# Performance work log

Measured on AMD Instinct MI355X. Metric: run time of the kernel, lower is better.

Reference implementation:

```python
import jax, jax.numpy as jnp
import numpy as np

B, N, C, H = 16, 4096, 256, 4
D = C // H

def setup_inputs() -> dict:
    key = jax.random.key(0)
    ks = jax.random.split(key, 8)
    w = 0.01  # small init, mimics xavier_uniform gain=0.1
    x = jax.random.normal(ks[0], (B, N, C), jnp.float32)
    S = jax.random.normal(ks[1], (B, H, D, D), jnp.float32) * 0.1
    Wq = jax.random.normal(ks[2], (C, C), jnp.float32) * w
    Wk = jax.random.normal(ks[3], (C, C), jnp.float32) * w
    Wv = jax.random.normal(ks[4], (C, C), jnp.float32) * w
    Wb = jax.random.normal(ks[5], (H, C), jnp.float32) * w  # beta_proj (zeros in torch init; random for nontrivial math)
    Wo = jax.random.normal(ks[6], (C, C), jnp.float32) * w
    g_rms = jnp.ones((C,), jnp.float32)
    return {"x": x, "S": S, "Wq": Wq, "Wk": Wk, "Wv": Wv, "Wb": Wb, "Wo": Wo, "g_rms": g_rms}

def reference(x, S, Wq, Wk, Wv, Wb, Wo, g_rms):
    b, n, c = x.shape
    h = Wb.shape[0]
    d = c // h
    # projections -> (B,H,N,D)
    q = (x @ Wq.T).reshape(b, n, h, d).transpose(0, 2, 1, 3)
    k = (x @ Wk.T).reshape(b, n, h, d).transpose(0, 2, 1, 3)
    v = (x @ Wv.T).reshape(b, n, h, d).transpose(0, 2, 1, 3)
    # feature map + L2 normalize keys
    k = jax.nn.elu(k) + 1.0
    k = k / (jnp.linalg.norm(k, axis=-1, keepdims=True) + 1e-6)
    # per-head gates (B,H,N,1)
    beta = jax.nn.sigmoid(jnp.einsum('bnc,hc->bhn', x, Wb))[..., None]
    # decay + state read
    Sd = S * 0.95
    y = jnp.einsum('bhij,bhnj->bhni', Sd, q)
    pred = jnp.einsum('bhij,bhnj->bhni', Sd, k)
    # delta-rule write: outer(mean weighted error, mean key)
    w_err = jnp.mean(beta * (v - pred), axis=2)  # (B,H,D)
    w_key = jnp.mean(k, axis=2)                  # (B,H,D)
    S_new = jnp.clip(Sd + jnp.einsum('bhi,bhj->bhij', w_err, w_key), -10.0, 10.0)
    # merge heads, RMSNorm, output projection
    y = y.transpose(0, 2, 1, 3).reshape(b, n, c)
    y = y * jax.lax.rsqrt(jnp.mean(y * y, axis=-1, keepdims=True) + 1e-6) * g_rms
    out = y @ Wo.T
    return out, S_new
```

## Files before the change

kernel.cpp:

```cpp
#include <hip/hip_runtime.h>
#include <math.h>


typedef _Float16 f16;
typedef f16 f16x8 __attribute__((ext_vector_type(8)));
typedef f16 f16x4 __attribute__((ext_vector_type(4)));
typedef float f32x4 __attribute__((ext_vector_type(4)));

__device__ __forceinline__ f16x8 cvt8(const float* q) {
  float4 a = *(const float4*)q;
  float4 b = *(const float4*)(q + 4);
  f16x8 r;
  r[0] = (f16)a.x; r[1] = (f16)a.y; r[2] = (f16)a.z; r[3] = (f16)a.w;
  r[4] = (f16)b.x; r[5] = (f16)b.y; r[6] = (f16)b.z; r[7] = (f16)b.w;
  return r;
}

__global__ __launch_bounds__(256) void prep_w(
    const float* __restrict__ Wk, const float* __restrict__ Wo,
    const float* __restrict__ g, f16* __restrict__ Wkh,
    f16* __restrict__ Wogh) {
  int i = blockIdx.x * 256 + threadIdx.x;
#pragma unroll
  for (int j = 0; j < 4; ++j) {
    int idx = i + j * 16384;
    Wkh[idx] = (f16)Wk[idx];
    Wogh[idx] = (f16)(Wo[idx] * g[idx & 255]);
  }
}

__global__ __launch_bounds__(256) void beta_xbsum_h(
    const float* __restrict__ x, const float* __restrict__ Wb,
    float* __restrict__ betaArr, float* __restrict__ xbsum,
    f16* __restrict__ xh) {
  const int t = threadIdx.x;
  const int wave = t >> 6, lane = t & 63;
  const int b = blockIdx.x >> 6;
  const int tile = blockIdx.x & 63;
  float4 wb[4];
#pragma unroll
  for (int h = 0; h < 4; ++h) wb[h] = *(const float4*)(Wb + h * 256 + lane * 4);
  float xacc[4][4] = {};
  const size_t rowbase = (size_t)b * 4096 + tile * 64;
  __shared__ float bsh[4][64];
  float4 xv = *(const float4*)(x + (rowbase + wave) * 256 + lane * 4);
#pragma unroll 2
  for (int i = 0; i < 16; ++i) {
    int r = i * 4 + wave;
    float4 nx = xv;
    if (i < 15)
      nx = *(const float4*)(x + (rowbase + r + 4) * 256 + lane * 4);
    f16x4 hx;
    hx[0] = (f16)xv.x; hx[1] = (f16)xv.y; hx[2] = (f16)xv.z; hx[3] = (f16)xv.w;
    *(f16x4*)(xh + (rowbase + r) * 256 + lane * 4) = hx;
#pragma unroll
    for (int h = 0; h < 4; ++h) {
      float s = xv.x * wb[h].x + xv.y * wb[h].y + xv.z * wb[h].z + xv.w * wb[h].w;
#pragma unroll
      for (int off = 32; off; off >>= 1) s += __shfl_xor(s, off);
      float bh = 1.f / (1.f + __expf(-s));
      if (lane == h) bsh[h][r] = bh;
      xacc[h][0] += bh * xv.x; xacc[h][1] += bh * xv.y;
      xacc[h][2] += bh * xv.z; xacc[h][3] += bh * xv.w;
    }
    xv = nx;
  }
  __shared__ float xbp[4][4][256];
#pragma unroll
  for (int h = 0; h < 4; ++h)
#pragma unroll
    for (int j = 0; j < 4; ++j) xbp[wave][h][lane * 4 + j] = xacc[h][j];
  __syncthreads();
  {
    int h = t >> 6, r = t & 63;
    betaArr[((size_t)(b * 4 + h) << 12) + tile * 64 + r] = bsh[h][r];
  }
  for (int idx = t; idx < 1024; idx += 256) {
    int h = idx >> 8, c = idx & 255;
    float s = xbp[0][h][c] + xbp[1][h][c] + xbp[2][h][c] + xbp[3][h][c];
    atomicAdd(&xbsum[(b * 4 + h) * 256 + c], s);
  }
}

__global__ __launch_bounds__(256) void kgemm_h(
    const f16* __restrict__ xh, const f16* __restrict__ Wkh,
    const float* __restrict__ betaArr,
    float* __restrict__ ksum, float* __restrict__ kbsum) {
  __shared__ union {
    struct { f16 A[128][72]; f16 B[128][72]; } s;
    f16 K[128][132];
  } u;
  __shared__ float bstage[2][128];
  const int t = threadIdx.x;
  const int m0 = blockIdx.y * 128;
  const int n0 = blockIdx.x * 128;
  const int b = m0 >> 12;
  const int wave = t >> 6, lane = t & 63;
  const int wm = (wave >> 1) * 64, wn = (wave & 1) * 64;
  const int fr = lane & 15, fq = lane >> 4;
  {
    int hh = t >> 7, r = t & 127;
    bstage[hh][r] =
        betaArr[((size_t)(b * 4 + (n0 >> 6) + hh) << 12) + (m0 & 4095) + r];
  }
  f32x4 acc[4][4] = {};
#pragma unroll 1
  for (int kt = 0; kt < 4; ++kt) {
    const int k0 = kt * 64;
#pragma unroll
    for (int i = 0; i < 4; ++i) {
      int id = i * 256 + t;
      int row = id >> 3, cc = id & 7;
      *(uint4*)&u.s.A[row][cc * 8] =
          *(const uint4*)(xh + (size_t)(m0 + row) * 256 + k0 + cc * 8);
      *(uint4*)&u.s.B[row][cc * 8] =
          *(const uint4*)(Wkh + (size_t)(n0 + row) * 256 + k0 + cc * 8);
    }
    __syncthreads();
#pragma unroll
    for (int ks = 0; ks < 2; ++ks) {
      f16x8 afr[4], bfr[4];
#pragma unroll
      for (int mi = 0; mi < 4; ++mi)
        afr[mi] = *(const f16x8*)&u.s.A[wm + mi * 16 + fr][ks * 32 + fq * 8];
#pragma unroll
      for (int ni = 0; ni < 4; ++ni)
        bfr[ni] = *(const f16x8*)&u.s.B[wn + ni * 16 + fr][ks * 32 + fq * 8];
#pragma unroll
      for (int mi = 0; mi < 4; ++mi)
#pragma unroll
        for (int ni = 0; ni < 4; ++ni)
          acc[mi][ni] = __builtin_amdgcn_mfma_f32_16x16x32_f16(
              afr[mi], bfr[ni], acc[mi][ni], 0, 0, 0);
    }
    __syncthreads();
  }
#pragma unroll
  for (int mi = 0; mi < 4; ++mi)
#pragma unroll
    for (int rr = 0; rr < 4; ++rr) {
      float s = 0.f;
#pragma unroll
      for (int ni = 0; ni < 4; ++ni) {
        float v = acc[mi][ni][rr];
        v = v > 0.f ? v + 1.f : __expf(v);
        acc[mi][ni][rr] = v;
        s += v * v;
      }
#pragma unroll
      for (int off = 1; off < 16; off <<= 1) s += __shfl_xor(s, off);
      float inv = 1.f / (sqrtf(s) + 1e-6f);
#pragma unroll
      for (int ni = 0; ni < 4; ++ni) acc[mi][ni][rr] *= inv;
    }
#pragma unroll
  for (int mi = 0; mi < 4; ++mi)
#pragma unroll
    for (int ni = 0; ni < 4; ++ni)
#pragma unroll
      for (int rr = 0; rr < 4; ++rr)
        u.K[wm + mi * 16 + fq * 4 + rr][wn + ni * 16 + fr] = (f16)acc[mi][ni][rr];
  __syncthreads();
  if (t < 128) {
    const int c = t, hl = c >> 6;
    float sk = 0.f, skb = 0.f;
#pragma unroll 4
    for (int r = 0; r < 128; ++r) {
      float v = (float)u.K[r][c];
      float be = bstage[hl][r];
      sk += v;
      skb += be * v;
    }
    int gh = b * 4 + (n0 >> 6) + hl;
    atomicAdd(&ksum[gh * 64 + (c & 63)], sk);
    atomicAdd(&kbsum[gh * 64 + (c & 63)], skb);
  }
}

__global__ __launch_bounds__(256) void fold_M(
    const float* __restrict__ S, const float* __restrict__ Wq,
    f16* __restrict__ M) {
  const int bh = blockIdx.y;
  const int dq = blockIdx.x;
  const int h = bh & 3;
  const int t = threadIdx.x;
  const float* Sp = S + (size_t)bh * 4096 + dq * 8 * 64;
  const float* Wp = Wq + (size_t)h * 64 * 256 + t;
  float m[8] = {};
#pragma unroll 4
  for (int e = 0; e < 64; ++e) {
    float wv = Wp[e * 256];
#pragma unroll
    for (int dd = 0; dd < 8; ++dd) m[dd] += Sp[dd * 64 + e] * wv;
  }
  f16* Mb = M + (size_t)(bh >> 2) * 65536;
#pragma unroll
  for (int dd = 0; dd < 8; ++dd)
    Mb[(size_t)(h * 64 + dq * 8 + dd) * 256 + t] = (f16)(0.95f * m[dd]);
}

__global__ __launch_bounds__(256) void ygemm_h(
    const f16* __restrict__ xh, int m_base, const f16* __restrict__ M,
    f16* __restrict__ y, float* __restrict__ rowssq) {
  __shared__ f16 As[128][72];
  __shared__ f16 Bs[128][72];
  const int t = threadIdx.x;
  const int m0 = blockIdx.y * 128;
  const int n0 = blockIdx.x * 128;
  const int b = (m_base + m0) >> 12;
  const f16* Mb = M + (size_t)b * 65536;
  const int wave = t >> 6, lane = t & 63;
  const int wm = (wave >> 1) * 64, wn = (wave & 1) * 64;
  const int fr = lane & 15, fq = lane >> 4;
  f32x4 acc[4][4] = {};
#pragma unroll 1
  for (int kt = 0; kt < 4; ++kt) {
    const int k0 = kt * 64;
#pragma unroll
    for (int i = 0; i < 4; ++i) {
      int id = i * 256 + t;
      int row = id >> 3, cc = id & 7;
      *(uint4*)&As[row][cc * 8] =
          *(const uint4*)(xh + (size_t)(m_base + m0 + row) * 256 + k0 + cc * 8);
      *(uint4*)&Bs[row][cc * 8] =
          *(const uint4*)(Mb + (size_t)(n0 + row) * 256 + k0 + cc * 8);
    }
    __syncthreads();
#pragma unroll
    for (int ks = 0; ks < 2; ++ks) {
      f16x8 afr[4], bfr[4];
#pragma unroll
      for (int mi = 0; mi < 4; ++mi)
        afr[mi] = *(const f16x8*)&As[wm + mi * 16 + fr][ks * 32 + fq * 8];
#pragma unroll
      for (int ni = 0; ni < 4; ++ni)
        bfr[ni] = *(const f16x8*)&Bs[wn + ni * 16 + fr][ks * 32 + fq * 8];
#pragma unroll
      for (int mi = 0; mi < 4; ++mi)
#pragma unroll
        for (int ni = 0; ni < 4; ++ni)
          acc[mi][ni] = __builtin_amdgcn_mfma_f32_16x16x32_f16(
              afr[mi], bfr[ni], acc[mi][ni], 0, 0, 0);
    }
    __syncthreads();
  }
#pragma unroll
  for (int mi = 0; mi < 4; ++mi)
#pragma unroll
    for (int rr = 0; rr < 4; ++rr) {
      float s = 0.f;
#pragma unroll
      for (int ni = 0; ni < 4; ++ni) {
        float v = acc[mi][ni][rr];
        s += v * v;
        int row = m0 + wm + mi * 16 + fq * 4 + rr;
        int col = n0 + wn + ni * 16 + fr;
        y[(size_t)row * 256 + col] = (f16)v;
      }
#pragma unroll
      for (int off = 1; off < 16; off <<= 1) s += __shfl_xor(s, off);
      if (fr == 0)
        atomicAdd(&rowssq[m0 + wm + mi * 16 + fq * 4 + rr], s);
    }
}

__global__ __launch_bounds__(256) void ogemm_h(
    const f16* __restrict__ y, const float* __restrict__ rowssq,
    const f16* __restrict__ Wogh, float* __restrict__ out, int m_base) {
  __shared__ f16 As[128][72];
  __shared__ f16 Bs[128][72];
  __shared__ float rsl[128];
  const int t = threadIdx.x;
  const int m0 = blockIdx.y * 128;
  const int n0 = blockIdx.x * 128;
  const int wave = t >> 6, lane = t & 63;
  const int wm = (wave >> 1) * 64, wn = (wave & 1) * 64;
  const int fr = lane & 15, fq = lane >> 4;
  if (t < 128) rsl[t] = rsqrtf(rowssq[m0 + t] * (1.f / 256.f) + 1e-6f);
  f32x4 acc[4][4] = {};
#pragma unroll 1
  for (int kt = 0; kt < 4; ++kt) {
    const int k0 = kt * 64;
#pragma unroll
    for (int i = 0; i < 4; ++i) {
      int id = i * 256 + t;
      int row = id >> 3, cc = id & 7;
      *(uint4*)&As[row][cc * 8] =
          *(const uint4*)(y + (size_t)(m0 + row) * 256 + k0 + cc * 8);
      *(uint4*)&Bs[row][cc * 8] =
          *(const uint4*)(Wogh + (size_t)(n0 + row) * 256 + k0 + cc * 8);
    }
    __syncthreads();
#pragma unroll
    for (int ks = 0; ks < 2; ++ks) {
      f16x8 afr[4], bfr[4];
#pragma unroll
      for (int mi = 0; mi < 4; ++mi)
        afr[mi] = *(const f16x8*)&As[wm + mi * 16 + fr][ks * 32 + fq * 8];
#pragma unroll
      for (int ni = 0; ni < 4; ++ni)
        bfr[ni] = *(const f16x8*)&Bs[wn + ni * 16 + fr][ks * 32 + fq * 8];
#pragma unroll
      for (int mi = 0; mi < 4; ++mi)
#pragma unroll
        for (int ni = 0; ni < 4; ++ni)
          acc[mi][ni] = __builtin_amdgcn_mfma_f32_16x16x32_f16(
              afr[mi], bfr[ni], acc[mi][ni], 0, 0, 0);
    }
    __syncthreads();
  }
#pragma unroll
  for (int mi = 0; mi < 4; ++mi)
#pragma unroll
    for (int rr = 0; rr < 4; ++rr) {
      int lrow = wm + mi * 16 + fq * 4 + rr;
      float rs = rsl[lrow];
#pragma unroll
      for (int ni = 0; ni < 4; ++ni) {
        int row = m_base + m0 + lrow;
        int col = n0 + wn + ni * 16 + fr;
        out[(size_t)row * 256 + col] = rs * acc[mi][ni][rr];
      }
    }
}

__global__ __launch_bounds__(256) void beta_xbsum(
    const float* __restrict__ x, const float* __restrict__ Wb,
    float* __restrict__ betaArr, float* __restrict__ xbsum) {
  const int t = threadIdx.x;
  const int wave = t >> 6, lane = t & 63;
  const int b = blockIdx.x >> 6;
  const int tile = blockIdx.x & 63;
  float4 wb[4];
#pragma unroll
  for (int h = 0; h < 4; ++h) wb[h] = *(const float4*)(Wb + h * 256 + lane * 4);
  float xacc[4][4] = {};
  const size_t rowbase = (size_t)b * 4096 + tile * 64;
  __shared__ float bsh[4][64];
  float4 xv = *(const float4*)(x + (rowbase + wave) * 256 + lane * 4);
#pragma unroll 2
  for (int i = 0; i < 16; ++i) {
    int r = i * 4 + wave;
    float4 nx = xv;
    if (i < 15)
      nx = *(const float4*)(x + (rowbase + r + 4) * 256 + lane * 4);
#pragma unroll
    for (int h = 0; h < 4; ++h) {
      float s = xv.x * wb[h].x + xv.y * wb[h].y + xv.z * wb[h].z + xv.w * wb[h].w;
#pragma unroll
      for (int off = 32; off; off >>= 1) s += __shfl_xor(s, off);
      float bh = 1.f / (1.f + __expf(-s));
      if (lane == h) bsh[h][r] = bh;
      xacc[h][0] += bh * xv.x; xacc[h][1] += bh * xv.y;
      xacc[h][2] += bh * xv.z; xacc[h][3] += bh * xv.w;
    }
    xv = nx;
  }
  __shared__ float xbp[4][4][256];
#pragma unroll
  for (int h = 0; h < 4; ++h)
#pragma unroll
    for (int j = 0; j < 4; ++j) xbp[wave][h][lane * 4 + j] = xacc[h][j];
  __syncthreads();
  {
    int h = t >> 6, r = t & 63;
    betaArr[((size_t)(b * 4 + h) << 12) + tile * 64 + r] = bsh[h][r];
  }
  for (int idx = t; idx < 1024; idx += 256) {
    int h = idx >> 8, c = idx & 255;
    float s = xbp[0][h][c] + xbp[1][h][c] + xbp[2][h][c] + xbp[3][h][c];
    atomicAdd(&xbsum[(b * 4 + h) * 256 + c], s);
  }
}

__global__ __launch_bounds__(256) void kgemm_sums(
    const float* __restrict__ x, const float* __restrict__ Wk,
    const float* __restrict__ betaArr,
    float* __restrict__ ksum, float* __restrict__ kbsum) {
  __shared__ union {
    struct { f16 A[128][72]; f16 B[128][72]; } s;
    f16 K[128][132];
  } u;
  __shared__ float bstage[2][128];
  const int t = threadIdx.x;
  const int m0 = blockIdx.y * 128;
  const int n0 = blockIdx.x * 128;
  const int b = m0 >> 12;
  const int wave = t >> 6, lane = t & 63;
  const int wm = (wave >> 1) * 64, wn = (wave & 1) * 64;
  const int fr = lane & 15, fq = lane >> 4;
  {
    int hh = t >> 7, r = t & 127;
    bstage[hh][r] =
        betaArr[((size_t)(b * 4 + (n0 >> 6) + hh) << 12) + (m0 & 4095) + r];
  }
  f32x4 acc[4][4] = {};
#pragma unroll 1
  for (int kt = 0; kt < 4; ++kt) {
    const int k0 = kt * 64;
#pragma unroll
    for (int i = 0; i < 4; ++i) {
      int id = i * 256 + t;
      int row = id >> 3, cc = id & 7;
      *(f16x8*)&u.s.A[row][cc * 8] =
          cvt8(x + (size_t)(m0 + row) * 256 + k0 + cc * 8);
      *(f16x8*)&u.s.B[row][cc * 8] =
          cvt8(Wk + (size_t)(n0 + row) * 256 + k0 + cc * 8);
    }
    __syncthreads();
#pragma unroll
    for (int ks = 0; ks < 2; ++ks) {
      f16x8 afr[4], bfr[4];
#pragma unroll
      for (int mi = 0; mi < 4; ++mi)
        afr[mi] = *(const f16x8*)&u.s.A[wm + mi * 16 + fr][ks * 32 + fq * 8];
#pragma unroll
      for (int ni = 0; ni < 4; ++ni)
        bfr[ni] = *(const f16x8*)&u.s.B[wn + ni * 16 + fr][ks * 32 + fq * 8];
#pragma unroll
      for (int mi = 0; mi < 4; ++mi)
#pragma unroll
        for (int ni = 0; ni < 4; ++ni)
          acc[mi][ni] = __builtin_amdgcn_mfma_f32_16x16x32_f16(
              afr[mi], bfr[ni], acc[mi][ni], 0, 0, 0);
    }
    __syncthreads();
  }
#pragma unroll
  for (int mi = 0; mi < 4; ++mi)
#pragma unroll
    for (int rr = 0; rr < 4; ++rr) {
      float s = 0.f;
#pragma unroll
      for (int ni = 0; ni < 4; ++ni) {
        float v = acc[mi][ni][rr];
        v = v > 0.f ? v + 1.f : __expf(v);
        acc[mi][ni][rr] = v;
        s += v * v;
      }
#pragma unroll
      for (int off = 1; off < 16; off <<= 1) s += __shfl_xor(s, off);
      float inv = 1.f / (sqrtf(s) + 1e-6f);
#pragma unroll
      for (int ni = 0; ni < 4; ++ni) acc[mi][ni][rr] *= inv;
    }
#pragma unroll
  for (int mi = 0; mi < 4; ++mi)
#pragma unroll
    for (int ni = 0; ni < 4; ++ni)
#pragma unroll
      for (int rr = 0; rr < 4; ++rr)
        u.K[wm + mi * 16 + fq * 4 + rr][wn + ni * 16 + fr] = (f16)acc[mi][ni][rr];
  __syncthreads();
  if (t < 128) {
    const int c = t, hl = c >> 6;
    float sk = 0.f, skb = 0.f;
#pragma unroll 4
    for (int r = 0; r < 128; ++r) {
      float v = (float)u.K[r][c];
      float be = bstage[hl][r];
      sk += v;
      skb += be * v;
    }
    int gh = b * 4 + (n0 >> 6) + hl;
    atomicAdd(&ksum[gh * 64 + (c & 63)], sk);
    atomicAdd(&kbsum[gh * 64 + (c & 63)], skb);
  }
}

__global__ __launch_bounds__(256) void ygemm_ssq(
    const float* __restrict__ x, int m_base, const f16* __restrict__ M,
    f16* __restrict__ y, float* __restrict__ rowssq) {
  __shared__ f16 As[128][72];
  __shared__ f16 Bs[128][72];
  const int t = threadIdx.x;
  const int m0 = blockIdx.y * 128;
  const int n0 = blockIdx.x * 128;
  const int b = (m_base + m0) >> 12;
  const f16* Mb = M + (size_t)b * 65536;
  const int wave = t >> 6, lane = t & 63;
  const int wm = (wave >> 1) * 64, wn = (wave & 1) * 64;
  const int fr = lane & 15, fq = lane >> 4;
  f32x4 acc[4][4] = {};
#pragma unroll 1
  for (int kt = 0; kt < 4; ++kt) {
    const int k0 = kt * 64;
#pragma unroll
    for (int i = 0; i < 4; ++i) {
      int id = i * 256 + t;
      int row = id >> 3, cc = id & 7;
      *(f16x8*)&As[row][cc * 8] =
          cvt8(x + (size_t)(m_base + m0 + row) * 256 + k0 + cc * 8);
      *(uint4*)&Bs[row][cc * 8] =
          *(const uint4*)(Mb + (size_t)(n0 + row) * 256 + k0 + cc * 8);
    }
    __syncthreads();
#pragma unroll
    for (int ks = 0; ks < 2; ++ks) {
      f16x8 afr[4], bfr[4];
#pragma unroll
      for (int mi = 0; mi < 4; ++mi)
        afr[mi] = *(const f16x8*)&As[wm + mi * 16 + fr][ks * 32 + fq * 8];
#pragma unroll
      for (int ni = 0; ni < 4; ++ni)
        bfr[ni] = *(const f16x8*)&Bs[wn + ni * 16 + fr][ks * 32 + fq * 8];
#pragma unroll
      for (int mi = 0; mi < 4; ++mi)
#pragma unroll
        for (int ni = 0; ni < 4; ++ni)
          acc[mi][ni] = __builtin_amdgcn_mfma_f32_16x16x32_f16(
              afr[mi], bfr[ni], acc[mi][ni], 0, 0, 0);
    }
    __syncthreads();
  }
#pragma unroll
  for (int mi = 0; mi < 4; ++mi)
#pragma unroll
    for (int rr = 0; rr < 4; ++rr) {
      float s = 0.f;
#pragma unroll
      for (int ni = 0; ni < 4; ++ni) {
        float v = acc[mi][ni][rr];
        s += v * v;
        int row = m0 + wm + mi * 16 + fq * 4 + rr;
        int col = n0 + wn + ni * 16 + fr;
        y[(size_t)row * 256 + col] = (f16)v;
      }
#pragma unroll
      for (int off = 1; off < 16; off <<= 1) s += __shfl_xor(s, off);
      if (fr == 0)
        atomicAdd(&rowssq[m0 + wm + mi * 16 + fq * 4 + rr], s);
    }
}

__global__ __launch_bounds__(256) void ogemm_scaled(
    const f16* __restrict__ y, const float* __restrict__ rowssq,
    const float* __restrict__ g_rms, const float* __restrict__ Wo,
    float* __restrict__ out, int m_base) {
  __shared__ f16 As[128][72];
  __shared__ f16 Bs[128][72];
  const int t = threadIdx.x;
  const int m0 = blockIdx.y * 128;
  const int n0 = blockIdx.x * 128;
  const int wave = t >> 6, lane = t & 63;
  const int wm = (wave >> 1) * 64, wn = (wave & 1) * 64;
  const int fr = lane & 15, fq = lane >> 4;
  f32x4 acc[4][4] = {};
#pragma unroll 1
  for (int kt = 0; kt < 4; ++kt) {
    const int k0 = kt * 64;
#pragma unroll
    for (int i = 0; i < 4; ++i) {
      int id = i * 256 + t;
      int row = id >> 3, cc = id & 7;
      float rs = rsqrtf(rowssq[m0 + row] * (1.f / 256.f) + 1e-6f);
      const f16* yp = y + (size_t)(m0 + row) * 256 + k0 + cc * 8;
      const float* gp = g_rms + k0 + cc * 8;
      f16x8 a;
#pragma unroll
      for (int j = 0; j < 8; ++j) a[j] = (f16)((float)yp[j] * rs * gp[j]);
      *(f16x8*)&As[row][cc * 8] = a;
      *(f16x8*)&Bs[row][cc * 8] =
          cvt8(Wo + (size_t)(n0 + row) * 256 + k0 + cc * 8);
    }
    __syncthreads();
#pragma unroll
    for (int ks = 0; ks < 2; ++ks) {
      f16x8 afr[4], bfr[4];
#pragma unroll
      for (int mi = 0; mi < 4; ++mi)
        afr[mi] = *(const f16x8*)&As[wm + mi * 16 + fr][ks * 32 + fq * 8];
#pragma unroll
      for (int ni = 0; ni < 4; ++ni)
        bfr[ni] = *(const f16x8*)&Bs[wn + ni * 16 + fr][ks * 32 + fq * 8];
#pragma unroll
      for (int mi = 0; mi < 4; ++mi)
#pragma unroll
        for (int ni = 0; ni < 4; ++ni)
          acc[mi][ni] = __builtin_amdgcn_mfma_f32_16x16x32_f16(
              afr[mi], bfr[ni], acc[mi][ni], 0, 0, 0);
    }
    __syncthreads();
  }
#pragma unroll
  for (int mi = 0; mi < 4; ++mi)
#pragma unroll
    for (int ni = 0; ni < 4; ++ni)
#pragma unroll
      for (int rr = 0; rr < 4; ++rr) {
        int row = m_base + m0 + wm + mi * 16 + fq * 4 + rr;
        int col = n0 + wn + ni * 16 + fr;
        out[(size_t)row * 256 + col] = acc[mi][ni][rr];
      }
}

__global__ __launch_bounds__(256) void finalize_S(
    const float* __restrict__ S, const float* __restrict__ Wv,
    const float* __restrict__ xbsum, const float* __restrict__ ksum,
    const float* __restrict__ kbsum, float* __restrict__ Sout) {
  const int bh = blockIdx.x;
  const int h = bh & 3;
  const int t = threadIdx.x;
  const int wave = t >> 6, lane = t & 63;
  __shared__ float xb[256], kb[64], key[64], errv[64];
  xb[t] = xbsum[bh * 256 + t];
  if (t < 64) {
    kb[t] = kbsum[bh * 64 + t];
    key[t] = ksum[bh * 64 + t] * (1.f / 4096.f);
  }
  __syncthreads();
#pragma unroll 1
  for (int ri = 0; ri < 16; ++ri) {
    int i = wave * 16 + ri;
    float4 wv4 = *(const float4*)(Wv + (size_t)(h * 64 + i) * 256 + lane * 4);
    float4 xb4 = *(const float4*)(&xb[lane * 4]);
    float s = wv4.x * xb4.x + wv4.y * xb4.y + wv4.z * xb4.z + wv4.w * xb4.w;
    s -= 0.95f * S[(size_t)bh * 4096 + i * 64 + lane] * kb[lane];
#pragma unroll
    for (int off = 32; off; off >>= 1) s += __shfl_xor(s, off);
    if (lane == 0) errv[i] = s * (1.f / 4096.f);
  }
  __syncthreads();
  for (int idx = t; idx < 4096; idx += 256) {
    int i = idx >> 6, j = idx & 63;
    float v = 0.95f * S[(size_t)bh * 4096 + idx] + errv[i] * key[j];
    Sout[(size_t)bh * 4096 + idx] = fminf(10.f, fmaxf(-10.f, v));
  }
}

extern "C" void kernel_launch(void* const* d_in, const int* in_sizes, int n_in,
                              void* d_out, int out_size, void* d_ws, size_t ws_size,
                              hipStream_t stream) {
  const float* x  = (const float*)d_in[0];
  const float* S  = (const float*)d_in[1];
  const float* Wq = (const float*)d_in[2];
  const float* Wk = (const float*)d_in[3];
  const float* Wv = (const float*)d_in[4];
  const float* Wb = (const float*)d_in[5];
  const float* Wo = (const float*)d_in[6];
  const float* g  = (const float*)d_in[7];

  char* w = (char*)d_ws;
  float* betaArr = (float*)w;
  f16*   M       = (f16*)(w + 1048576);
  f16*   y       = (f16*)(w + 3145728);
  float* rowssq  = (float*)(w + 19922944);
  float* xbsum   = (float*)(w + 20185088);
  float* ksum    = (float*)(w + 20250624);
  float* kbsum   = (float*)(w + 20267008);
  f16*   xh      = (f16*)(w + 20283392);
  f16*   Wkh     = (f16*)(w + 53837824);
  f16*   Wogh    = (f16*)(w + 53968896);
  const size_t WS_NEED = 54099968ull;

  float* out  = (float*)d_out;
  float* Sout = out + (size_t)16 * 4096 * 256;

  hipMemsetAsync(w + 19922944, 0, 360448, stream);

  if (ws_size >= WS_NEED) {
    prep_w<<<64, 256, 0, stream>>>(Wk, Wo, g, Wkh, Wogh);
    beta_xbsum_h<<<1024, 256, 0, stream>>>(x, Wb, betaArr, xbsum, xh);
    kgemm_h<<<dim3(2, 512), 256, 0, stream>>>(xh, Wkh, betaArr, ksum, kbsum);
    fold_M<<<dim3(8, 64), 256, 0, stream>>>(S, Wq, M);
    for (int half = 0; half < 2; ++half) {
      int m_base = half * 32768;
      ygemm_h<<<dim3(2, 256), 256, 0, stream>>>(xh, m_base, M, y,
                                                rowssq + half * 32768);
      ogemm_h<<<dim3(2, 256), 256, 0, stream>>>(y, rowssq + half * 32768,
                                                Wogh, out, m_base);
    }
  } else {
    beta_xbsum<<<1024, 256, 0, stream>>>(x, Wb, betaArr, xbsum);
    kgemm_sums<<<dim3(2, 512), 256, 0, stream>>>(x, Wk, betaArr, ksum, kbsum);
    fold_M<<<dim3(8, 64), 256, 0, stream>>>(S, Wq, M);
    for (int half = 0; half < 2; ++half) {
      int m_base = half * 32768;
      ygemm_ssq<<<dim3(2, 256), 256, 0, stream>>>(x, m_base, M, y,
                                                  rowssq + half * 32768);
      ogemm_scaled<<<dim3(2, 256), 256, 0, stream>>>(y, rowssq + half * 32768,
                                                     g, Wo, out, m_base);
    }
  }
  finalize_S<<<64, 256, 0, stream>>>(S, Wv, xbsum, ksum, kbsum, Sout);
}
```

Measured before the change: 235.8 us.

## Load GEMM tiles via direct global-to-LDS loads with XOR-swizzled layout

Replaces the register-staged global-to-shared tile copies in the three f16 MFMA GEMM kernels (kgemm_h, ygemm_h, ogemm_h) with global_load_lds direct loads. The shared tiles drop their padding and use an XOR swizzle on 16-byte chunks, so fragment reads stay free of bank conflicts. This is meant to cut VGPR traffic and instruction count in the load phase and shrink LDS use. The kgemm_h union's K[128][128] epilogue buffer also loses its padding, which could add bank conflicts there, and the correctness of the swizzle mapping depends on the per-wave LDS placement semantics of the builtin.

```diff
diff --git a/kernel.cpp b/kernel.cpp
--- a/kernel.cpp
+++ b/kernel.cpp
@@ -6,6 +6,13 @@
 typedef f16 f16x8 __attribute__((ext_vector_type(8)));
 typedef f16 f16x4 __attribute__((ext_vector_type(4)));
 typedef float f32x4 __attribute__((ext_vector_type(4)));
+
+typedef const __attribute__((address_space(1))) void gvoid;
+typedef __attribute__((address_space(3))) void svoid;
+
+__device__ __forceinline__ void gload16(const void* g, void* l) {
+  __builtin_amdgcn_global_load_lds((gvoid*)g, (svoid*)l, 16, 0, 0);
+}
 
 __device__ __forceinline__ f16x8 cvt8(const float* q) {
   float4 a = *(const float4*)q;
@@ -87,8 +94,8 @@
     const float* __restrict__ betaArr,
     float* __restrict__ ksum, float* __restrict__ kbsum) {
   __shared__ union {
-    struct { f16 A[128][72]; f16 B[128][72]; } s;
-    f16 K[128][132];
+    struct { f16 A[128][64]; f16 B[128][64]; } s;
+    f16 K[128][128];
   } u;
   __shared__ float bstage[2][128];
   const int t = threadIdx.x;
@@ -98,34 +105,38 @@
   const int wave = t >> 6, lane = t & 63;
   const int wm = (wave >> 1) * 64, wn = (wave & 1) * 64;
   const int fr = lane & 15, fq = lane >> 4;
+  const int fr7 = fr & 7;
+  const int srow = lane >> 3;
+  const int sc = (lane & 7) ^ srow;
   {
     int hh = t >> 7, r = t & 127;
     bstage[hh][r] =
         betaArr[((size_t)(b * 4 + (n0 >> 6) + hh) << 12) + (m0 & 4095) + r];
   }
+  const char* Ab = (const char*)&u.s.A[0][0];
+  const char* Bb = (const char*)&u.s.B[0][0];
   f32x4 acc[4][4] = {};
 #pragma unroll 1
   for (int kt = 0; kt < 4; ++kt) {
     const int k0 = kt * 64;
 #pragma unroll
-    for (int i = 0; i < 4; ++i) {
-      int id = i * 256 + t;
-      int row = id >> 3, cc = id & 7;
-      *(uint4*)&u.s.A[row][cc * 8] =
-          *(const uint4*)(xh + (size_t)(m0 + row) * 256 + k0 + cc * 8);
-      *(uint4*)&u.s.B[row][cc * 8] =
-          *(const uint4*)(Wkh + (size_t)(n0 + row) * 256 + k0 + cc * 8);
+    for (int j = 0; j < 4; ++j) {
+      int c = j * 4 + wave;
+      int row = c * 8 + srow;
+      gload16(xh + (size_t)(m0 + row) * 256 + k0 + sc * 8, &u.s.A[0][0] + c * 512);
+      gload16(Wkh + (size_t)(n0 + row) * 256 + k0 + sc * 8, &u.s.B[0][0] + c * 512);
     }
     __syncthreads();
 #pragma unroll
     for (int ks = 0; ks < 2; ++ks) {
+      const int p = ((ks * 4 + fq) ^ fr7) << 4;
       f16x8 afr[4], bfr[4];
 #pragma unroll
       for (int mi = 0; mi < 4; ++mi)
-        afr[mi] = *(const f16x8*)&u.s.A[wm + mi * 16 + fr][ks * 32 + fq * 8];
+        afr[mi] = *(const f16x8*)(Ab + (wm + mi * 16 + fr) * 128 + p);
 #pragma unroll
       for (int ni = 0; ni < 4; ++ni)
-        bfr[ni] = *(const f16x8*)&u.s.B[wn + ni * 16 + fr][ks * 32 + fq * 8];
+        bfr[ni] = *(const f16x8*)(Bb + (wn + ni * 16 + fr) * 128 + p);
 #pragma unroll
       for (int mi = 0; mi < 4; ++mi)
 #pragma unroll
@@ -202,8 +213,8 @@
 __global__ __launch_bounds__(256) void ygemm_h(
     const f16* __restrict__ xh, int m_base, const f16* __restrict__ M,
     f16* __restrict__ y, float* __restrict__ rowssq) {
-  __shared__ f16 As[128][72];
-  __shared__ f16 Bs[128][72];
+  __shared__ f16 As[128][64];
+  __shared__ f16 Bs[128][64];
   const int t = threadIdx.x;
   const int m0 = blockIdx.y * 128;
   const int n0 = blockIdx.x * 128;
@@ -212,29 +223,34 @@
   const int wave = t >> 6, lane = t & 63;
   const int wm = (wave >> 1) * 64, wn = (wave & 1) * 64;
   const int fr = lane & 15, fq = lane >> 4;
+  const int fr7 = fr & 7;
+  const int srow = lane >> 3;
+  const int sc = (lane & 7) ^ srow;
+  const char* Ab = (const char*)&As[0][0];
+  const char* Bb = (const char*)&Bs[0][0];
   f32x4 acc[4][4] = {};
 #pragma unroll 1
   for (int kt = 0; kt < 4; ++kt) {
     const int k0 = kt * 64;
 #pragma unroll
-    for (int i = 0; i < 4; ++i) {
-      int id = i * 256 + t;
-      int row = id >> 3, cc = id & 7;
-      *(uint4*)&As[row][cc * 8] =
-          *(const uint4*)(xh + (size_t)(m_base + m0 + row) * 256 + k0 + cc * 8);
-      *(uint4*)&Bs[row][cc * 8] =
-          *(const uint4*)(Mb + (size_t)(n0 + row) * 256 + k0 + cc * 8);
+    for (int j = 0; j < 4; ++j) {
+      int c = j * 4 + wave;
+      int row = c * 8 + srow;
+      gload16(xh + (size_t)(m_base + m0 + row) * 256 + k0 + sc * 8,
+              &As[0][0] + c * 512);
+      gload16(Mb + (size_t)(n0 + row) * 256 + k0 + sc * 8, &Bs[0][0] + c * 512);
     }
     __syncthreads();
 #pragma unroll
     for (int ks = 0; ks < 2; ++ks) {
+      const int p = ((ks * 4 + fq) ^ fr7) << 4;
       f16x8 afr[4], bfr[4];
 #pragma unroll
       for (int mi = 0; mi < 4; ++mi)
-        afr[mi] = *(const f16x8*)&As[wm + mi * 16 + fr][ks * 32 + fq * 8];
+        afr[mi] = *(const f16x8*)(Ab + (wm + mi * 16 + fr) * 128 + p);
 #pragma unroll
       for (int ni = 0; ni < 4; ++ni)
-        bfr[ni] = *(const f16x8*)&Bs[wn + ni * 16 + fr][ks * 32 + fq * 8];
+        bfr[ni] = *(const f16x8*)(Bb + (wn + ni * 16 + fr) * 128 + p);
 #pragma unroll
       for (int mi = 0; mi < 4; ++mi)
 #pragma unroll
@@ -267,8 +283,8 @@
 __global__ __launch_bounds__(256) void ogemm_h(
     const f16* __restrict__ y, const float* __restrict__ rowssq,
     const f16* __restrict__ Wogh, float* __restrict__ out, int m_base) {
-  __shared__ f16 As[128][72];
-  __shared__ f16 Bs[128][72];
+  __shared__ f16 As[128][64];
+  __shared__ f16 Bs[128][64];
   __shared__ float rsl[128];
   const int t = threadIdx.x;
   const int m0 = blockIdx.y * 128;
@@ -276,30 +292,34 @@
   const int wave = t >> 6, lane = t & 63;
   const int wm = (wave >> 1) * 64, wn = (wave & 1) * 64;
   const int fr = lane & 15, fq = lane >> 4;
+  const int fr7 = fr & 7;
+  const int srow = lane >> 3;
+  const int sc = (lane & 7) ^ srow;
+  const char* Ab = (const char*)&As[0][0];
+  const char* Bb = (const char*)&Bs[0][0];
   if (t < 128) rsl[t] = rsqrtf(rowssq[m0 + t] * (1.f / 256.f) + 1e-6f);
   f32x4 acc[4][4] = {};
 #pragma unroll 1
   for (int kt = 0; kt < 4; ++kt) {
     const int k0 = kt * 64;
 #pragma unroll
-    for (int i = 0; i < 4; ++i) {
-      int id = i * 256 + t;
-      int row = id >> 3, cc = id & 7;
-      *(uint4*)&As[row][cc * 8] =
-          *(const uint4*)(y + (size_t)(m0 + row) * 256 + k0 + cc * 8);
-      *(uint4*)&Bs[row][cc * 8] =
-          *(const uint4*)(Wogh + (size_t)(n0 + row) * 256 + k0 + cc * 8);
+    for (int j = 0; j < 4; ++j) {
+      int c = j * 4 + wave;
+      int row = c * 8 + srow;
+      gload16(y + (size_t)(m0 + row) * 256 + k0 + sc * 8, &As[0][0] + c * 512);
+      gload16(Wogh + (size_t)(n0 + row) * 256 + k0 + sc * 8, &Bs[0][0] + c * 512);
     }
     __syncthreads();
 #pragma unroll
     for (int ks = 0; ks < 2; ++ks) {
+      const int p = ((ks * 4 + fq) ^ fr7) << 4;
       f16x8 afr[4], bfr[4];
 #pragma unroll
       for (int mi = 0; mi < 4; ++mi)
-        afr[mi] = *(const f16x8*)&As[wm + mi * 16 + fr][ks * 32 + fq * 8];
+        afr[mi] = *(const f16x8*)(Ab + (wm + mi * 16 + fr) * 128 + p);
 #pragma unroll
       for (int ni = 0; ni < 4; ++ni)
-        bfr[ni] = *(const f16x8*)&Bs[wn + ni * 16 + fr][ks * 32 + fq * 8];
+        bfr[ni] = *(const f16x8*)(Bb + (wn + ni * 16 + fr) * 128 + p);
 #pragma unroll
       for (int mi = 0; mi < 4; ++mi)
 #pragma unroll
```

After: 235.0 us. No clear change (-0.4%).
